# Performance work log

Measured on AMD Instinct MI355X. Metric: run time of the kernel, lower is better.

The kernel has to match this reference:

```python
import jax, jax.numpy as jnp
import numpy as np
import math

S, B, D, H = 1024, 4, 1024, 16
DH = D // H


def setup_inputs() -> dict:
    key = jax.random.key(0)
    ks = jax.random.split(key, 8)
    hidden_states = jax.random.normal(ks[0], (S, B, D), dtype=jnp.float32)
    u = jax.random.uniform(ks[1], (B, 1, 1, S), dtype=jnp.float32)
    attention_mask = jnp.where(u < 0.2, jnp.float32(-10000.0), jnp.float32(0.0))
    std = 0.02
    Wq = jax.random.normal(ks[2], (D, D), dtype=jnp.float32) * std
    bq = jnp.zeros((D,), dtype=jnp.float32)
    Wk = jax.random.normal(ks[3], (D, D), dtype=jnp.float32) * std
    bk = jnp.zeros((D,), dtype=jnp.float32)
    Wv = jax.random.normal(ks[4], (D, D), dtype=jnp.float32) * std
    bv = jnp.zeros((D,), dtype=jnp.float32)
    return {"hidden_states": hidden_states, "attention_mask": attention_mask,
            "Wq": Wq, "bq": bq, "Wk": Wk, "bk": bk, "Wv": Wv, "bv": bv}


def _split_heads(x):
    # [S,B,D] -> [B,H,S,DH]
    s, b, d = x.shape
    return x.reshape(s, b, H, DH).transpose(1, 2, 0, 3)


def reference(hidden_states, attention_mask, Wq, bq, Wk, bk, Wv, bv):
    scale = 1.0 / math.sqrt(DH)
    q = _split_heads(hidden_states @ Wq.T + bq)  # [B,H,S,DH]
    k = _split_heads(hidden_states @ Wk.T + bk)
    v = _split_heads(hidden_states @ Wv.T + bv)
    # scaled scores + additive mask (mask [B,1,1,S] broadcasts over heads, query pos)
    scores = jnp.einsum('bhsd,bhtd->bhst', q, k) * scale + attention_mask  # [B,H,S,S]
    probs = jax.nn.softmax(scores, axis=-1)
    # NOTE: original forward's dropout block is a no-op (only reshapes), so none applied
    ctx = jnp.einsum('bhst,bhtd->bhsd', probs, v)  # [B,H,S,DH]
    # -> [S,B,D]
    return ctx.transpose(2, 0, 1, 3).reshape(S, B, D)
```

## Files before the change

### kernel.cpp

```cpp
#include <hip/hip_runtime.h>
#include <hip/hip_bf16.h>

#define S_LEN  1024
#define BATCH  4
#define DMODEL 1024
#define NHEAD  16
#define DHEAD  64
#define NROWS  (S_LEN*BATCH)

typedef __bf16 bf16;
typedef __bf16 bf16x2 __attribute__((ext_vector_type(2)));
typedef __bf16 bf16x4 __attribute__((ext_vector_type(4)));
typedef __bf16 bf16x8 __attribute__((ext_vector_type(8)));
typedef float  f32x4  __attribute__((ext_vector_type(4)));
typedef float  f32x16 __attribute__((ext_vector_type(16)));

#define AS1 __attribute__((address_space(1)))
#define AS3 __attribute__((address_space(3)))

#define QSCALE  0.18033688011112042f

__device__ __forceinline__ void gload16(const bf16* g, bf16* l) {
  __builtin_amdgcn_global_load_lds((const AS1 void*)g, (AS3 void*)l, 16, 0, 0);
}

__device__ __forceinline__ float fast_exp2(float x) {
#if __has_builtin(__builtin_amdgcn_exp2f)
  return __builtin_amdgcn_exp2f(x);
#else
  return exp2f(x);
#endif
}

__global__ __launch_bounds__(256) void cvt_all(
    const float* __restrict__ hs, const float* __restrict__ wq,
    const float* __restrict__ wk, const float* __restrict__ wv,
    bf16* __restrict__ Xb, bf16* __restrict__ Wb)
{
  const int b = blockIdx.x;
  const float* src; bf16* dst; int i;
  if (b < 2048)      { src = hs; dst = Xb;                           i = b*256        + threadIdx.x; }
  else if (b < 2560) { src = wq; dst = Wb;                           i = (b-2048)*256 + threadIdx.x; }
  else if (b < 3072) { src = wk; dst = Wb + (size_t)DMODEL*DMODEL;   i = (b-2560)*256 + threadIdx.x; }
  else               { src = wv; dst = Wb + (size_t)2*DMODEL*DMODEL; i = (b-3072)*256 + threadIdx.x; }
  const float4* s4 = (const float4*)src;
  float4 a = s4[2*i], c = s4[2*i+1];
  bf16x8 o;
  o[0]=(bf16)a.x; o[1]=(bf16)a.y; o[2]=(bf16)a.z; o[3]=(bf16)a.w;
  o[4]=(bf16)c.x; o[5]=(bf16)c.y; o[6]=(bf16)c.z; o[7]=(bf16)c.w;
  ((bf16x8*)dst)[i] = o;
}

#define BM 128
#define BN 128
#define BK 32

__global__ __launch_bounds__(256) void qkv_gemm(
    const bf16* __restrict__ X, const bf16* __restrict__ Wcat,
    const float* __restrict__ bq, const float* __restrict__ bk, const float* __restrict__ bv,
    bf16* __restrict__ Qo, bf16* __restrict__ Ko, bf16* __restrict__ Vo)
{
  __shared__ __align__(16) bf16 As[BM*BK];
  __shared__ __align__(16) bf16 Bs[BN*BK];

  const int tid  = threadIdx.x;
  const int row0 = blockIdx.x * BM;
  const int col0 = blockIdx.y * BN;
  const int wsel = col0 >> 10;
  const int coln = col0 & 1023;

  const int wv   = tid >> 6;
  const int lane = tid & 63;
  const int lg   = lane >> 4;
  const int lr   = lane & 15;
  const int wr   = (wv >> 1) << 6;
  const int wc   = (wv & 1) << 6;

  const int c0 = tid, c1 = tid + 256;
  const size_t gA0 = (size_t)(row0 + (c0>>2))*DMODEL + (size_t)((c0&3)<<3);
  const size_t gA1 = (size_t)(row0 + (c1>>2))*DMODEL + (size_t)((c1&3)<<3);
  const size_t gB0 = (size_t)(col0 + (c0>>2))*DMODEL + (size_t)((c0&3)<<3);
  const size_t gB1 = (size_t)(col0 + (c1>>2))*DMODEL + (size_t)((c1&3)<<3);
  const int wb = (tid >> 6) << 6;
  bf16* lA0 = As + (size_t)wb*8;
  bf16* lA1 = As + (size_t)(wb+256)*8;
  bf16* lB0 = Bs + (size_t)wb*8;
  bf16* lB1 = Bs + (size_t)(wb+256)*8;

  f32x4 acc[4][4];
  #pragma unroll
  for (int mi=0; mi<4; ++mi)
    #pragma unroll
    for (int ni=0; ni<4; ++ni)
      acc[mi][ni] = (f32x4){0.f,0.f,0.f,0.f};

  for (int k0 = 0; k0 < DMODEL; k0 += BK) {
    __syncthreads();
    gload16(X    + gA0 + k0, lA0);
    gload16(X    + gA1 + k0, lA1);
    gload16(Wcat + gB0 + k0, lB0);
    gload16(Wcat + gB1 + k0, lB1);
    __syncthreads();

    bf16x8 af[4], bfr[4];
    #pragma unroll
    for (int mi=0; mi<4; ++mi)
      af[mi] = *(const bf16x8*)&As[(wr + mi*16 + lr)*BK + lg*8];
    #pragma unroll
    for (int ni=0; ni<4; ++ni)
      bfr[ni] = *(const bf16x8*)&Bs[(wc + ni*16 + lr)*BK + lg*8];

    #pragma unroll
    for (int mi=0; mi<4; ++mi)
      #pragma unroll
      for (int ni=0; ni<4; ++ni)
        acc[mi][ni] = __builtin_amdgcn_mfma_f32_16x16x32_bf16(af[mi], bfr[ni], acc[mi][ni], 0, 0, 0);
  }

  const float* bias = (wsel==0) ? bq : ((wsel==1) ? bk : bv);
  bf16* Out = (wsel==0) ? Qo : ((wsel==1) ? Ko : Vo);
  const float oscale = (wsel==0) ? QSCALE : 1.0f;

  #pragma unroll
  for (int ni=0; ni<4; ++ni) {
    const int co = coln + wc + ni*16 + lr;
    const float bias_v = bias[co];
    const int h  = co >> 6;
    const int dh = co & 63;
    #pragma unroll
    for (int mi=0; mi<4; ++mi) {
      #pragma unroll
      for (int p=0; p<4; ++p) {
        const int gr = row0 + wr + mi*16 + lg*4 + p;
        const int s_ = gr >> 2;
        const int b_ = gr & 3;
        Out[((size_t)(b_*NHEAD + h)*S_LEN + s_)*DHEAD + dh] = (bf16)((acc[mi][ni][p] + bias_v) * oscale);
      }
    }
  }
}

#define QBLK 128
#define LSW(row, chunk) (((row)<<6) + ((((chunk) ^ ((row)&7)))<<3))

__global__ __launch_bounds__(256, 2) void attn_mfma(
    const bf16* __restrict__ Q, const bf16* __restrict__ K, const bf16* __restrict__ V,
    const float* __restrict__ mask, float* __restrict__ out)
{
  __shared__ __align__(16) bf16 Ks[2][64*64];
  __shared__ __align__(16) bf16 Vt[2][64*64];
  __shared__ float Mskf[S_LEN];
  __shared__ float Linv[4][32];

  const int bh   = blockIdx.x;
  const int b_   = bh >> 4;
  const int h_   = bh & 15;
  const int tid  = threadIdx.x;
  const int wv   = tid >> 6;
  const int lane = tid & 63;
  const int l31  = lane & 31;
  const int hh   = lane >> 5;
  const int q0   = blockIdx.y * QBLK;

  *(float4*)&Mskf[tid*4] = *(const float4*)&mask[(size_t)b_*S_LEN + tid*4];

  const bf16* Qp = Q + ((size_t)bh*S_LEN + q0 + wv*32 + l31)*DHEAD;
  bf16x8 qb[4];
  #pragma unroll
  for (int dk=0; dk<4; ++dk) qb[dk] = *(const bf16x8*)&Qp[dk*16 + hh*8];

  const bf16* Kb = K + (size_t)bh*S_LEN*DHEAD;
  const bf16* Vb = V + (size_t)bh*S_LEN*DHEAD;

  const int krow = tid >> 2, kch = tid & 3;
  const int vrow = tid & 63, vcb = tid >> 6;

  bf16x8 kr0 = *(const bf16x8*)&Kb[(size_t)krow*DHEAD + kch*8];
  bf16x8 kr1 = *(const bf16x8*)&Kb[(size_t)krow*DHEAD + kch*8 + 32];
  bf16x8 vr0 = *(const bf16x8*)&Vb[(size_t)vrow*DHEAD + vcb*16];
  bf16x8 vr1 = *(const bf16x8*)&Vb[(size_t)vrow*DHEAD + vcb*16 + 8];
  {
    *(bf16x8*)&Ks[0][LSW(krow, kch)]   = kr0;
    *(bf16x8*)&Ks[0][LSW(krow, kch+4)] = kr1;
    #pragma unroll
    for (int i=0;i<8;++i) {
      const int d0 = vcb*16 + i, d1 = d0 + 8;
      Vt[0][(d0<<6) + (((vrow>>3) ^ (d0&7))<<3) + (vrow&7)] = vr0[i];
      Vt[0][(d1<<6) + (((vrow>>3) ^ (d1&7))<<3) + (vrow&7)] = vr1[i];
    }
  }
  __syncthreads();

  f32x16 ctx[2];
  ctx[0] = (f32x16)0.f; ctx[1] = (f32x16)0.f;
  float lsum = 0.f;

  for (int t = 0; t < 16; ++t) {
    const bf16* Kc = Ks[t & 1];
    const bf16* Vc = Vt[t & 1];

    if (t < 15) {
      const size_t nb = (size_t)(t+1)*64;
      kr0 = *(const bf16x8*)&Kb[(nb+krow)*DHEAD + kch*8];
      kr1 = *(const bf16x8*)&Kb[(nb+krow)*DHEAD + kch*8 + 32];
      vr0 = *(const bf16x8*)&Vb[(nb+vrow)*DHEAD + vcb*16];
      vr1 = *(const bf16x8*)&Vb[(nb+vrow)*DHEAD + vcb*16 + 8];
    }

    f32x16 sacc[2];
    sacc[0] = (f32x16)0.f; sacc[1] = (f32x16)0.f;
    __builtin_amdgcn_s_setprio(1);
    #pragma unroll
    for (int tt=0; tt<2; ++tt) {
      const int row = tt*32 + l31;
      #pragma unroll
      for (int dk=0; dk<4; ++dk) {
        bf16x8 ka = *(const bf16x8*)&Kc[LSW(row, dk*2 + hh)];
        sacc[tt] = __builtin_amdgcn_mfma_f32_32x32x16_bf16(ka, qb[dk], sacc[tt], 0,0,0);
      }
    }
    __builtin_amdgcn_s_setprio(0);

    const int tb = t*64;
    bf16x8 pf[2][2];
    #pragma unroll
    for (int tt=0; tt<2; ++tt) {
      f32x4 mv[4];
      #pragma unroll
      for (int g=0; g<4; ++g)
        mv[g] = *(const f32x4*)&Mskf[tb + tt*32 + 8*g + 4*hh];
      float pe[16];
      #pragma unroll
      for (int e=0; e<16; ++e) {
        pe[e] = fast_exp2(sacc[tt][e] + mv[e>>2][e&3]);
        lsum += pe[e];
      }
      union { bf16x2 h2[8]; bf16x8 v[2]; } u;
      #pragma unroll
      for (int j=0; j<8; ++j) { bf16x2 p2; p2[0]=(bf16)pe[2*j]; p2[1]=(bf16)pe[2*j+1]; u.h2[j]=p2; }
      pf[tt][0] = u.v[0]; pf[tt][1] = u.v[1];
    }

    __builtin_amdgcn_s_setprio(1);
    #pragma unroll
    for (int nt=0; nt<2; ++nt) {
      const int drow = nt*32 + l31;
      const int dbase = (drow<<6) + 4*hh;
      const int dsw = (drow&7);
      #pragma unroll
      for (int tt=0; tt<2; ++tt) {
        #pragma unroll
        for (int kk=0; kk<2; ++kk) {
          const int lc = tt*4 + kk*2;
          bf16x4 lo = *(const bf16x4*)&Vc[dbase + (((lc  ) ^ dsw)<<3)];
          bf16x4 hi = *(const bf16x4*)&Vc[dbase + (((lc+1) ^ dsw)<<3)];
          bf16x8 vb;
          #pragma unroll
          for (int j=0; j<4; ++j) { vb[j]=lo[j]; vb[4+j]=hi[j]; }
          ctx[nt] = __builtin_amdgcn_mfma_f32_32x32x16_bf16(pf[tt][kk], vb, ctx[nt], 0,0,0);
        }
      }
    }
    __builtin_amdgcn_s_setprio(0);

    if (t < 15) {
      bf16* Kn = (bf16*)Ks[(t+1) & 1];
      bf16* Vn = (bf16*)Vt[(t+1) & 1];
      *(bf16x8*)&Kn[LSW(krow, kch)]   = kr0;
      *(bf16x8*)&Kn[LSW(krow, kch+4)] = kr1;
      #pragma unroll
      for (int i=0;i<8;++i) {
        const int d0 = vcb*16 + i, d1 = d0 + 8;
        Vn[(d0<<6) + (((vrow>>3) ^ (d0&7))<<3) + (vrow&7)] = vr0[i];
        Vn[(d1<<6) + (((vrow>>3) ^ (d1&7))<<3) + (vrow&7)] = vr1[i];
      }
    }
    __syncthreads();
  }

  const float tot = lsum + __shfl_xor(lsum, 32);
  if (lane < 32) Linv[wv][l31] = 1.f / tot;
  f32x4 inv4[4];
  #pragma unroll
  for (int g4=0; g4<4; ++g4) inv4[g4] = *(const f32x4*)&Linv[wv][8*g4 + 4*hh];

  float* op = out + ((size_t)(q0 + wv*32)*BATCH + b_)*DMODEL + h_*DHEAD + l31;
  #pragma unroll
  for (int e=0; e<16; ++e) {
    const int qe = (e&3) + 8*(e>>2) + 4*hh;
    const float inv = inv4[e>>2][e&3];
    float* oq = op + (size_t)qe*BATCH*DMODEL;
    oq[0]  = ctx[0][e] * inv;
    oq[32] = ctx[1][e] * inv;
  }
}

extern "C" void kernel_launch(void* const* d_in, const int* in_sizes, int n_in,
                              void* d_out, int out_size, void* d_ws, size_t ws_size,
                              hipStream_t stream) {
  const float* hs   = (const float*)d_in[0];
  const float* mask = (const float*)d_in[1];
  const float* Wq   = (const float*)d_in[2];
  const float* bq   = (const float*)d_in[3];
  const float* Wk   = (const float*)d_in[4];
  const float* bk   = (const float*)d_in[5];
  const float* Wv   = (const float*)d_in[6];
  const float* bv   = (const float*)d_in[7];
  float* out = (float*)d_out;

  char* ws = (char*)d_ws;
  bf16* Xb = (bf16*)ws;
  bf16* Wb = Xb + (size_t)NROWS*DMODEL;
  bf16* Qw = Wb + (size_t)3*DMODEL*DMODEL;
  bf16* Kw = Qw + (size_t)NROWS*DMODEL;
  bf16* Vw = Kw + (size_t)NROWS*DMODEL;

  cvt_all<<<3584, 256, 0, stream>>>(hs, Wq, Wk, Wv, Xb, Wb);

  qkv_gemm<<<dim3(NROWS/BM, 3*DMODEL/BN), 256, 0, stream>>>(Xb, Wb, bq, bk, bv, Qw, Kw, Vw);

  attn_mfma<<<dim3(BATCH*NHEAD, S_LEN/QBLK), 256, 0, stream>>>(Qw, Kw, Vw, mask, out);
}
```

Before: 71.16 us.

## Software-pipeline QK and softmax-PV halves with triple-buffered K/V tiles

Moves the K/V shared-memory staging from a double buffer to a triple buffer with a two-tile-ahead prefetch. The loop is split into half-tiles so the QK MFMA of the next half can overlap the exp/PV work of the current half. The mask is folded in by initialising the score accumulator with it, and the row sum is kept in four partial accumulators. This raises LDS use to 48KB+ per block, which may limit occupancy at two blocks per CU, and adds register pressure from the extra live score tile.

After: 72.21 us. Within noise of the previous version (+1.5%).

```diff
diff --git a/kernel.cpp b/kernel.cpp
--- a/kernel.cpp
+++ b/kernel.cpp
@@ -147,8 +147,8 @@
     const bf16* __restrict__ Q, const bf16* __restrict__ K, const bf16* __restrict__ V,
     const float* __restrict__ mask, float* __restrict__ out)
 {
-  __shared__ __align__(16) bf16 Ks[2][64*64];
-  __shared__ __align__(16) bf16 Vt[2][64*64];
+  __shared__ __align__(16) bf16 Ks[3][64*64];
+  __shared__ __align__(16) bf16 Vt[3][64*64];
   __shared__ float Mskf[S_LEN];
   __shared__ float Linv[4][32];
 
@@ -175,72 +175,57 @@
   const int krow = tid >> 2, kch = tid & 3;
   const int vrow = tid & 63, vcb = tid >> 6;
 
-  bf16x8 kr0 = *(const bf16x8*)&Kb[(size_t)krow*DHEAD + kch*8];
-  bf16x8 kr1 = *(const bf16x8*)&Kb[(size_t)krow*DHEAD + kch*8 + 32];
-  bf16x8 vr0 = *(const bf16x8*)&Vb[(size_t)vrow*DHEAD + vcb*16];
-  bf16x8 vr1 = *(const bf16x8*)&Vb[(size_t)vrow*DHEAD + vcb*16 + 8];
-  {
-    *(bf16x8*)&Ks[0][LSW(krow, kch)]   = kr0;
-    *(bf16x8*)&Ks[0][LSW(krow, kch+4)] = kr1;
+  bf16x8 kr0, kr1, vr0, vr1;
+
+  auto stage_load = [&](int t) {
+    const size_t nb = (size_t)t*64;
+    kr0 = *(const bf16x8*)&Kb[(nb+krow)*DHEAD + kch*8];
+    kr1 = *(const bf16x8*)&Kb[(nb+krow)*DHEAD + kch*8 + 32];
+    vr0 = *(const bf16x8*)&Vb[(nb+vrow)*DHEAD + vcb*16];
+    vr1 = *(const bf16x8*)&Vb[(nb+vrow)*DHEAD + vcb*16 + 8];
+  };
+  auto stage_write = [&](bf16* Kd, bf16* Vd) {
+    *(bf16x8*)&Kd[LSW(krow, kch)]   = kr0;
+    *(bf16x8*)&Kd[LSW(krow, kch+4)] = kr1;
     #pragma unroll
     for (int i=0;i<8;++i) {
       const int d0 = vcb*16 + i, d1 = d0 + 8;
-      Vt[0][(d0<<6) + (((vrow>>3) ^ (d0&7))<<3) + (vrow&7)] = vr0[i];
-      Vt[0][(d1<<6) + (((vrow>>3) ^ (d1&7))<<3) + (vrow&7)] = vr1[i];
-    }
-  }
-  __syncthreads();
+      Vd[(d0<<6) + (((vrow>>3) ^ (d0&7))<<3) + (vrow&7)] = vr0[i];
+      Vd[(d1<<6) + (((vrow>>3) ^ (d1&7))<<3) + (vrow&7)] = vr1[i];
+    }
+  };
 
   f32x16 ctx[2];
   ctx[0] = (f32x16)0.f; ctx[1] = (f32x16)0.f;
-  float lsum = 0.f;
-
-  for (int t = 0; t < 16; ++t) {
-    const bf16* Kc = Ks[t & 1];
-    const bf16* Vc = Vt[t & 1];
-
-    if (t < 15) {
-      const size_t nb = (size_t)(t+1)*64;
-      kr0 = *(const bf16x8*)&Kb[(nb+krow)*DHEAD + kch*8];
-      kr1 = *(const bf16x8*)&Kb[(nb+krow)*DHEAD + kch*8 + 32];
-      vr0 = *(const bf16x8*)&Vb[(nb+vrow)*DHEAD + vcb*16];
-      vr1 = *(const bf16x8*)&Vb[(nb+vrow)*DHEAD + vcb*16 + 8];
-    }
-
-    f32x16 sacc[2];
-    sacc[0] = (f32x16)0.f; sacc[1] = (f32x16)0.f;
+  f32x4 lsum4 = (f32x4){0.f,0.f,0.f,0.f};
+
+  auto qk_half = [&](f32x16& s, const bf16* Kbuf, int mbase, int tt) {
+    #pragma unroll
+    for (int g4=0; g4<4; ++g4) {
+      const f32x4 m4 = *(const f32x4*)&Mskf[mbase + 8*g4 + 4*hh];
+      s[4*g4+0]=m4[0]; s[4*g4+1]=m4[1]; s[4*g4+2]=m4[2]; s[4*g4+3]=m4[3];
+    }
+    const int row = tt*32 + l31;
     __builtin_amdgcn_s_setprio(1);
     #pragma unroll
-    for (int tt=0; tt<2; ++tt) {
-      const int row = tt*32 + l31;
-      #pragma unroll
-      for (int dk=0; dk<4; ++dk) {
-        bf16x8 ka = *(const bf16x8*)&Kc[LSW(row, dk*2 + hh)];
-        sacc[tt] = __builtin_amdgcn_mfma_f32_32x32x16_bf16(ka, qb[dk], sacc[tt], 0,0,0);
-      }
+    for (int dk=0; dk<4; ++dk) {
+      bf16x8 ka = *(const bf16x8*)&Kbuf[LSW(row, dk*2 + hh)];
+      s = __builtin_amdgcn_mfma_f32_32x32x16_bf16(ka, qb[dk], s, 0,0,0);
     }
     __builtin_amdgcn_s_setprio(0);
-
-    const int tb = t*64;
-    bf16x8 pf[2][2];
-    #pragma unroll
-    for (int tt=0; tt<2; ++tt) {
-      f32x4 mv[4];
-      #pragma unroll
-      for (int g=0; g<4; ++g)
-        mv[g] = *(const f32x4*)&Mskf[tb + tt*32 + 8*g + 4*hh];
-      float pe[16];
-      #pragma unroll
-      for (int e=0; e<16; ++e) {
-        pe[e] = fast_exp2(sacc[tt][e] + mv[e>>2][e&3]);
-        lsum += pe[e];
-      }
+  };
+
+  auto sm_pv = [&](const f32x16& s, const bf16* Vc, int tt) {
+    float pe[16];
+    #pragma unroll
+    for (int e=0; e<16; ++e) { pe[e] = fast_exp2(s[e]); lsum4[e&3] += pe[e]; }
+    bf16x8 pf[2];
+    {
       union { bf16x2 h2[8]; bf16x8 v[2]; } u;
       #pragma unroll
       for (int j=0; j<8; ++j) { bf16x2 p2; p2[0]=(bf16)pe[2*j]; p2[1]=(bf16)pe[2*j+1]; u.h2[j]=p2; }
-      pf[tt][0] = u.v[0]; pf[tt][1] = u.v[1];
-    }
-
+      pf[0] = u.v[0]; pf[1] = u.v[1];
+    }
     __builtin_amdgcn_s_setprio(1);
     #pragma unroll
     for (int nt=0; nt<2; ++nt) {
@@ -248,36 +233,46 @@
       const int dbase = (drow<<6) + 4*hh;
       const int dsw = (drow&7);
       #pragma unroll
-      for (int tt=0; tt<2; ++tt) {
+      for (int kk=0; kk<2; ++kk) {
+        const int lc = tt*4 + kk*2;
+        bf16x4 lo = *(const bf16x4*)&Vc[dbase + (((lc  ) ^ dsw)<<3)];
+        bf16x4 hi = *(const bf16x4*)&Vc[dbase + (((lc+1) ^ dsw)<<3)];
+        bf16x8 vb;
         #pragma unroll
-        for (int kk=0; kk<2; ++kk) {
-          const int lc = tt*4 + kk*2;
-          bf16x4 lo = *(const bf16x4*)&Vc[dbase + (((lc  ) ^ dsw)<<3)];
-          bf16x4 hi = *(const bf16x4*)&Vc[dbase + (((lc+1) ^ dsw)<<3)];
-          bf16x8 vb;
-          #pragma unroll
-          for (int j=0; j<4; ++j) { vb[j]=lo[j]; vb[4+j]=hi[j]; }
-          ctx[nt] = __builtin_amdgcn_mfma_f32_32x32x16_bf16(pf[tt][kk], vb, ctx[nt], 0,0,0);
-        }
+        for (int j=0; j<4; ++j) { vb[j]=lo[j]; vb[4+j]=hi[j]; }
+        ctx[nt] = __builtin_amdgcn_mfma_f32_32x32x16_bf16(pf[kk], vb, ctx[nt], 0,0,0);
       }
     }
     __builtin_amdgcn_s_setprio(0);
-
-    if (t < 15) {
-      bf16* Kn = (bf16*)Ks[(t+1) & 1];
-      bf16* Vn = (bf16*)Vt[(t+1) & 1];
-      *(bf16x8*)&Kn[LSW(krow, kch)]   = kr0;
-      *(bf16x8*)&Kn[LSW(krow, kch+4)] = kr1;
-      #pragma unroll
-      for (int i=0;i<8;++i) {
-        const int d0 = vcb*16 + i, d1 = d0 + 8;
-        Vn[(d0<<6) + (((vrow>>3) ^ (d0&7))<<3) + (vrow&7)] = vr0[i];
-        Vn[(d1<<6) + (((vrow>>3) ^ (d1&7))<<3) + (vrow&7)] = vr1[i];
-      }
-    }
+  };
+
+  stage_load(0);
+  stage_write(&Ks[0][0], &Vt[0][0]);
+  stage_load(1);
+  __syncthreads();
+  stage_write(&Ks[1][0], &Vt[1][0]);
+
+  f32x16 sA, sB;
+  qk_half(sA, &Ks[0][0], 0, 0);
+  __syncthreads();
+
+  for (int t = 0; t < 16; ++t) {
+    const bf16* Kc = &Ks[t%3][0];
+    const bf16* Vc = &Vt[t%3][0];
+
+    if (t < 14) stage_load(t+2);
+
+    qk_half(sB, Kc, t*64 + 32, 1);
+    sm_pv(sA, Vc, 0);
+
+    if (t < 15) qk_half(sA, &Ks[(t+1)%3][0], (t+1)*64, 0);
+    sm_pv(sB, Vc, 1);
+
+    if (t < 14) stage_write(&Ks[(t+2)%3][0], &Vt[(t+2)%3][0]);
     __syncthreads();
   }
 
+  float lsum = (lsum4[0] + lsum4[1]) + (lsum4[2] + lsum4[3]);
   const float tot = lsum + __shfl_xor(lsum, 32);
   if (lane < 32) Linv[wv][l31] = 1.f / tot;
   f32x4 inv4[4];
```
